# Kernel tuning notes

Measured on AMD Instinct MI355X. Metric: run time of the kernel, lower is better.

Reference implementation:

```python
import jax, jax.numpy as jnp
import numpy as np

N = 50000      # nodes
E = 800000     # edges (avg degree 16)
SIZES = [128, 128, 128, 128, 64]
NUM_LAYERS = 4


def setup_inputs() -> dict:
    key = jax.random.key(0)
    ks = jax.random.split(key, 3 + 2 * NUM_LAYERS)
    inp = {
        "x": jax.random.normal(ks[0], (N, SIZES[0]), dtype=jnp.float32),
        "edge_index": jax.random.randint(ks[1], (2, E), 0, N, dtype=jnp.int64),
        "edge_weight": jax.random.uniform(ks[2], (E,), dtype=jnp.float32),
    }
    for i in range(NUM_LAYERS):
        fan_in = SIZES[i]
        inp[f"W{i}"] = (jax.random.normal(ks[3 + 2 * i], (SIZES[i], SIZES[i + 1]), dtype=jnp.float32)
                        / np.float32(np.sqrt(fan_in)))
        inp[f"b{i}"] = jnp.zeros((SIZES[i + 1],), dtype=jnp.float32)
    return inp


def gcn_conv(x, src, dst, ew, W, b, n):
    """PyG GCNConv with add_self_loops=True, normalize=True (eval mode).
    deg[i] = sum of incoming edge weights at i + 1 (self loop weight 1).
    norm(j->i) = deg[j]^-1/2 * w_ji * deg[i]^-1/2.
    Self loop contributes deg[i]^-1 * (xW)[i].
    """
    xw = x @ W                                                    # [n, out]
    deg = jax.ops.segment_sum(ew, dst, num_segments=n) + 1.0      # [n]
    dinv = jnp.where(deg > 0, jax.lax.rsqrt(deg), 0.0)            # deg^-1/2
    norm = dinv[src] * ew * dinv[dst]                             # [E]
    agg = jax.ops.segment_sum(xw[src] * norm[:, None], dst, num_segments=n)
    return agg + xw * (dinv * dinv)[:, None] + b


def reference(x, edge_index, edge_weight, W0, b0, W1, b1, W2, b2, W3, b3):
    # Dropout p=0.5 is identity in eval mode (training=False).
    src, dst = edge_index[0], edge_index[1]
    Ws = [W0, W1, W2, W3]
    bs = [b0, b1, b2, b3]
    for i in range(NUM_LAYERS):
        x = gcn_conv(x, src, dst, edge_weight, Ws[i], bs[i], N)
        if i < NUM_LAYERS - 1:
            x = jax.nn.relu(x)
    return x
```

## Files before the change

kernel.cpp:

```cpp
#include <hip/hip_runtime.h>
#include <hip/hip_fp16.h>


#define DEG_SCALE 4194304.0f
#define BCAP 5120
#define K1_EDGES 4096
#define ACT_LD 136

using f16x8 = __attribute__((ext_vector_type(8))) _Float16;
using f32x4 = __attribute__((ext_vector_type(4))) float;

__global__ void prep_kernel(const float* __restrict__ W0, const float* __restrict__ W1,
                            const float* __restrict__ W2, const float* __restrict__ W3,
                            __half* P0, __half* P1, __half* P2, __half* P3,
                            int* gCursor, int nBuckets) {
    int blk = blockIdx.x;
    if (blk == 28) {
        int t = threadIdx.x;
        if (t < nBuckets) gCursor[t] = t * BCAP;
        return;
    }
    int t = blk * 256 + threadIdx.x;
    const float* W;
    __half* P;
    int OUT;
    if (t < 2048)      { W = W0; P = P0; OUT = 128; }
    else if (t < 4096) { W = W1; P = P1; OUT = 128; t -= 2048; }
    else if (t < 6144) { W = W2; P = P2; OUT = 128; t -= 4096; }
    else               { W = W3; P = P3; OUT = 64;  t -= 6144; }
    int lane = t & 63, fi = t >> 6;
    int nt = fi >> 2, kc = fi & 3;
    int col = 16 * nt + (lane & 15);
    int k0  = 32 * kc + 8 * (lane >> 4);
    union { __half h[8]; uint4 u; } v;
#pragma unroll
    for (int j = 0; j < 8; j++) v.h[j] = __float2half_rn(W[(size_t)(k0 + j) * OUT + col]);
    *(uint4*)&P[((size_t)fi * 64 + lane) * 8] = v.u;
}

__global__ __launch_bounds__(256) void bucket_scatter_kernel(
        const int* __restrict__ src, const int* __restrict__ dst,
        const float* __restrict__ ew, int* gCursor,
        int2* __restrict__ bucketArr, int E, int nBuckets) {
    __shared__ int cnt[256];
    __shared__ int runBase[256];
    int tid = threadIdx.x;
    int e0 = blockIdx.x * K1_EDGES;
    int e1 = min(e0 + K1_EDGES, E);
    cnt[tid] = 0;
    __syncthreads();
    for (int e = e0 + tid; e < e1; e += 256)
        atomicAdd(&cnt[dst[e] >> 8], 1);
    __syncthreads();
    if (tid < nBuckets && cnt[tid] > 0)
        runBase[tid] = atomicAdd(&gCursor[tid], cnt[tid]);
    __syncthreads();
    cnt[tid] = 0;
    __syncthreads();
    for (int e = e0 + tid; e < e1; e += 256) {
        int d = dst[e];
        int b = d >> 8;
        int slot = runBase[b] + atomicAdd(&cnt[b], 1);
        if (slot < (b + 1) * BCAP)
            bucketArr[slot] = make_int2((src[e] & 0xFFFF) | (d << 16),
                                        __float_as_int(ew[e]));
    }
}

__global__ __launch_bounds__(256) void bucket_csr_kernel(
        const int2* __restrict__ bucketArr, const int* __restrict__ gCursor,
        int2* __restrict__ epack, int* __restrict__ row_ptr,
        float* __restrict__ dinv, int N, int E, int nBuckets) {
    __shared__ int2 st[BCAP];
    __shared__ int cnt[256];
    __shared__ int scn[256];
    __shared__ int cur[256];
    __shared__ unsigned int dfix[256];
    __shared__ int cbase_sh;
    int b   = blockIdx.x;
    int tid = threadIdx.x;
    int node0 = b << 8;
    int nloc  = min(256, N - node0);
    int base  = b * BCAP;

    int sz = (tid < nBuckets) ? (gCursor[tid] - tid * BCAP) : 0;
    scn[tid] = sz;
    __syncthreads();
    for (int off = 1; off < 256; off <<= 1) {
        int u = (tid >= off) ? scn[tid - off] : 0;
        __syncthreads();
        scn[tid] += u;
        __syncthreads();
    }
    if (tid == b) cbase_sh = scn[tid] - sz;
    cnt[tid]  = 0;
    dfix[tid] = 0u;
    __syncthreads();
    int cbase = cbase_sh;
    int size  = gCursor[b] - base;

    for (int i = tid; i < size; i += 256) {
        int2 v = bucketArr[base + i];
        st[i] = v;
        int dl = (v.x >> 16) & 255;
        atomicAdd(&cnt[dl], 1);
        atomicAdd(&dfix[dl], (unsigned int)rintf(__int_as_float(v.y) * DEG_SCALE));
    }
    __syncthreads();

    if (tid < nloc) {
        float d = (float)dfix[tid] * (1.0f / DEG_SCALE) + 1.0f;
        dinv[node0 + tid] = rsqrtf(d);
    }

    int val = cnt[tid];
    scn[tid] = val;
    __syncthreads();
    for (int off = 1; off < 256; off <<= 1) {
        int u = (tid >= off) ? scn[tid - off] : 0;
        __syncthreads();
        scn[tid] += u;
        __syncthreads();
    }
    int excl = scn[tid] - val;
    scn[tid] = excl;
    if (tid < nloc) row_ptr[node0 + tid] = cbase + excl;
    if (b == nBuckets - 1 && tid == 0) row_ptr[N] = E;
    cur[tid] = 0;
    __syncthreads();

    for (int i = tid; i < size; i += 256) {
        int2 v = st[i];
        int dl = (v.x >> 16) & 255;
        int p  = cbase + scn[dl] + atomicAdd(&cur[dl], 1);
        epack[p] = make_int2(v.x & 0xFFFF, v.y);
    }
}

__global__ __launch_bounds__(256) void gemm0_kernel(const float* __restrict__ x,
                                                    const __half* __restrict__ Wpack,
                                                    const float* __restrict__ dinv,
                                                    __half* __restrict__ xw, int nrows) {
    constexpr int OUT = 128, NT = 8, CPR = 16;
    __shared__ __half D[64 * OUT];
    int tid  = threadIdx.x;
    int wave = tid >> 6, lane = tid & 63;
    int r = lane & 15, g = lane >> 4;
    int row0 = blockIdx.x * 64 + wave * 16;

    int arow = row0 + r;
    if (arow >= nrows) arow = nrows - 1;

    f16x8 a[4];
#pragma unroll
    for (int kc = 0; kc < 4; kc++) {
        const float* p = x + (size_t)arow * 128 + kc * 32 + g * 8;
        float4 u = *(const float4*)p;
        float4 v = *(const float4*)(p + 4);
        a[kc][0] = (_Float16)u.x; a[kc][1] = (_Float16)u.y;
        a[kc][2] = (_Float16)u.z; a[kc][3] = (_Float16)u.w;
        a[kc][4] = (_Float16)v.x; a[kc][5] = (_Float16)v.y;
        a[kc][6] = (_Float16)v.z; a[kc][7] = (_Float16)v.w;
    }

    float4 dv = *(const float4*)&dinv[row0 + 4 * g];

#pragma unroll
    for (int nt = 0; nt < NT; nt++) {
        const f16x8* Bp = (const f16x8*)(Wpack) + (size_t)nt * 4 * 64 + lane;
        f32x4 c = {0.f, 0.f, 0.f, 0.f};
        c = __builtin_amdgcn_mfma_f32_16x16x32_f16(a[0], Bp[0],   c, 0, 0, 0);
        c = __builtin_amdgcn_mfma_f32_16x16x32_f16(a[1], Bp[64],  c, 0, 0, 0);
        c = __builtin_amdgcn_mfma_f32_16x16x32_f16(a[2], Bp[128], c, 0, 0, 0);
        c = __builtin_amdgcn_mfma_f32_16x16x32_f16(a[3], Bp[192], c, 0, 0, 0);
        c[0] *= dv.x; c[1] *= dv.y; c[2] *= dv.z; c[3] *= dv.w;
        int col = 16 * nt + r;
#pragma unroll
        for (int j = 0; j < 4; j++) {
            int drow = wave * 16 + 4 * g + j;
            int ch   = (col >> 3) ^ (drow & (CPR - 1));
            D[drow * OUT + ch * 8 + (col & 7)] = __float2half_rn(c[j]);
        }
    }
    __syncthreads();
#pragma unroll
    for (int i = 0; i < 4; i++) {
        int idx  = tid + i * 256;
        int drow = idx / CPR;
        int ch   = idx % CPR;
        int gr   = blockIdx.x * 64 + drow;
        if (gr < nrows) {
            f16x8 v = *(f16x8*)&D[drow * OUT + ((ch ^ (drow & (CPR - 1))) << 3)];
            *(f16x8*)&xw[(size_t)gr * OUT + ch * 8] = v;
        }
    }
}

template <int OUT_NEXT>
__global__ __launch_bounds__(256) void gather_gemm_kernel(
        const __half* __restrict__ xwh,
        const int* __restrict__ rp,
        const int2* __restrict__ epack,
        const float* __restrict__ dinv,
        const float* __restrict__ bias,
        const __half* __restrict__ Wpack,
        __half* __restrict__ xw_out,
        int n) {
    constexpr int NT  = OUT_NEXT / 16;
    constexpr int CPR = OUT_NEXT / 8;
    __shared__ __half actAll[4 * 16 * ACT_LD];
    int tid  = threadIdx.x;
    int wv   = tid >> 6, lane = tid & 63;
    __half* act = &actAll[wv * 16 * ACT_LD];
    int node0 = blockIdx.x * 64 + wv * 16;

    for (int lrow = 0; lrow < 16; lrow++) {
        int node = node0 + lrow;
        if (node >= n) continue;
        node = __builtin_amdgcn_readfirstlane(node);
        int e0 = rp[node], e1 = rp[node + 1];
        float ax = 0.f, ay = 0.f;
        int e = e0;
        for (; e + 8 <= e1; e += 8) {
            int2 v0 = epack[e + 0], v1 = epack[e + 1], v2 = epack[e + 2], v3 = epack[e + 3];
            int2 v4 = epack[e + 4], v5 = epack[e + 5], v6 = epack[e + 6], v7 = epack[e + 7];
            __half2 h0 = ((const __half2*)(xwh + (size_t)v0.x * 128))[lane];
            __half2 h1 = ((const __half2*)(xwh + (size_t)v1.x * 128))[lane];
            __half2 h2 = ((const __half2*)(xwh + (size_t)v2.x * 128))[lane];
            __half2 h3 = ((const __half2*)(xwh + (size_t)v3.x * 128))[lane];
            __half2 h4 = ((const __half2*)(xwh + (size_t)v4.x * 128))[lane];
            __half2 h5 = ((const __half2*)(xwh + (size_t)v5.x * 128))[lane];
            __half2 h6 = ((const __half2*)(xwh + (size_t)v6.x * 128))[lane];
            __half2 h7 = ((const __half2*)(xwh + (size_t)v7.x * 128))[lane];
            float w0 = __int_as_float(v0.y), w1 = __int_as_float(v1.y);
            float w2 = __int_as_float(v2.y), w3 = __int_as_float(v3.y);
            float w4 = __int_as_float(v4.y), w5 = __int_as_float(v5.y);
            float w6 = __int_as_float(v6.y), w7 = __int_as_float(v7.y);
            ax += __half2float(h0.x) * w0 + __half2float(h1.x) * w1
                + __half2float(h2.x) * w2 + __half2float(h3.x) * w3
                + __half2float(h4.x) * w4 + __half2float(h5.x) * w5
                + __half2float(h6.x) * w6 + __half2float(h7.x) * w7;
            ay += __half2float(h0.y) * w0 + __half2float(h1.y) * w1
                + __half2float(h2.y) * w2 + __half2float(h3.y) * w3
                + __half2float(h4.y) * w4 + __half2float(h5.y) * w5
                + __half2float(h6.y) * w6 + __half2float(h7.y) * w7;
        }
        for (; e + 2 <= e1; e += 2) {
            int2 v0 = epack[e + 0], v1 = epack[e + 1];
            __half2 h0 = ((const __half2*)(xwh + (size_t)v0.x * 128))[lane];
            __half2 h1 = ((const __half2*)(xwh + (size_t)v1.x * 128))[lane];
            float w0 = __int_as_float(v0.y), w1 = __int_as_float(v1.y);
            ax += __half2float(h0.x) * w0 + __half2float(h1.x) * w1;
            ay += __half2float(h0.y) * w0 + __half2float(h1.y) * w1;
        }
        for (; e < e1; e++) {
            int2 v = epack[e];
            __half2 h = ((const __half2*)(xwh + (size_t)v.x * 128))[lane];
            float w = __int_as_float(v.y);
            ax += __half2float(h.x) * w;
            ay += __half2float(h.y) * w;
        }
        float   dvn = dinv[node];
        __half2 hs  = ((const __half2*)(xwh + (size_t)node * 128))[lane];
        float2  bl  = *(const float2*)&bias[lane * 2];
        float ox = fmaxf(dvn * (ax + __half2float(hs.x)) + bl.x, 0.f);
        float oy = fmaxf(dvn * (ay + __half2float(hs.y)) + bl.y, 0.f);
        __half2 ho;
        ho.x = __float2half_rn(ox);
        ho.y = __float2half_rn(oy);
        *(__half2*)&act[lrow * ACT_LD + lane * 2] = ho;
    }

    int r = lane & 15, g = lane >> 4;
    f16x8 a[4];
#pragma unroll
    for (int kc = 0; kc < 4; kc++)
        a[kc] = *(const f16x8*)&act[r * ACT_LD + kc * 32 + g * 8];

    float4 dvw = *(const float4*)&dinv[node0 + 4 * g];

#pragma unroll
    for (int nt = 0; nt < NT; nt++) {
        const f16x8* Bp = (const f16x8*)(Wpack) + (size_t)nt * 4 * 64 + lane;
        f32x4 c = {0.f, 0.f, 0.f, 0.f};
        c = __builtin_amdgcn_mfma_f32_16x16x32_f16(a[0], Bp[0],   c, 0, 0, 0);
        c = __builtin_amdgcn_mfma_f32_16x16x32_f16(a[1], Bp[64],  c, 0, 0, 0);
        c = __builtin_amdgcn_mfma_f32_16x16x32_f16(a[2], Bp[128], c, 0, 0, 0);
        c = __builtin_amdgcn_mfma_f32_16x16x32_f16(a[3], Bp[192], c, 0, 0, 0);
        c[0] *= dvw.x; c[1] *= dvw.y; c[2] *= dvw.z; c[3] *= dvw.w;
        int col = 16 * nt + r;
#pragma unroll
        for (int j = 0; j < 4; j++) {
            int drow = 4 * g + j;
            int ch   = (col >> 3) ^ (drow & (CPR - 1));
            act[drow * OUT_NEXT + ch * 8 + (col & 7)] = __float2half_rn(c[j]);
        }
    }

#pragma unroll
    for (int i = 0; i < 16 * CPR / 64; i++) {
        int idx  = lane + i * 64;
        int drow = idx / CPR;
        int ch   = idx % CPR;
        int gr   = node0 + drow;
        if (gr < n) {
            f16x8 v = *(f16x8*)&act[drow * OUT_NEXT + ((ch ^ (drow & (CPR - 1))) << 3)];
            *(f16x8*)&xw_out[(size_t)gr * OUT_NEXT + ch * 8] = v;
        }
    }
}

__global__ __launch_bounds__(256) void gather64h_kernel(const __half* __restrict__ xwh,
                                                        const int* __restrict__ rp,
                                                        const int2* __restrict__ epack,
                                                        const float* __restrict__ dinv,
                                                        const float* __restrict__ bias,
                                                        float* __restrict__ out, int n) {
    int lane = threadIdx.x & 63;
    int node = (blockIdx.x * blockDim.x + threadIdx.x) >> 6;
    if (node >= n) return;
    node = __builtin_amdgcn_readfirstlane(node);
    int e0 = rp[node], e1 = rp[node + 1];
    float acc = 0.f;

    int e = e0;
    for (; e + 8 <= e1; e += 8) {
        int2 v0 = epack[e + 0], v1 = epack[e + 1], v2 = epack[e + 2], v3 = epack[e + 3];
        int2 v4 = epack[e + 4], v5 = epack[e + 5], v6 = epack[e + 6], v7 = epack[e + 7];
        float r0 = __half2float(xwh[(size_t)v0.x * 64 + lane]);
        float r1 = __half2float(xwh[(size_t)v1.x * 64 + lane]);
        float r2 = __half2float(xwh[(size_t)v2.x * 64 + lane]);
        float r3 = __half2float(xwh[(size_t)v3.x * 64 + lane]);
        float r4 = __half2float(xwh[(size_t)v4.x * 64 + lane]);
        float r5 = __half2float(xwh[(size_t)v5.x * 64 + lane]);
        float r6 = __half2float(xwh[(size_t)v6.x * 64 + lane]);
        float r7 = __half2float(xwh[(size_t)v7.x * 64 + lane]);
        acc += r0 * __int_as_float(v0.y) + r1 * __int_as_float(v1.y)
             + r2 * __int_as_float(v2.y) + r3 * __int_as_float(v3.y)
             + r4 * __int_as_float(v4.y) + r5 * __int_as_float(v5.y)
             + r6 * __int_as_float(v6.y) + r7 * __int_as_float(v7.y);
    }
    for (; e < e1; e++) {
        int2 v = epack[e];
        acc += __half2float(xwh[(size_t)v.x * 64 + lane]) * __int_as_float(v.y);
    }

    float self = __half2float(xwh[(size_t)node * 64 + lane]);
    out[(size_t)node * 64 + lane] = dinv[node] * (acc + self) + bias[lane];
}

extern "C" void kernel_launch(void* const* d_in, const int* in_sizes, int n_in,
                              void* d_out, int out_size, void* d_ws, size_t ws_size,
                              hipStream_t stream) {
    const float* x  = (const float*)d_in[0];
    const int*   ei = (const int*)d_in[1];
    const float* ew = (const float*)d_in[2];
    const float* W[4] = {(const float*)d_in[3], (const float*)d_in[5],
                         (const float*)d_in[7], (const float*)d_in[9]};
    const float* b[4] = {(const float*)d_in[4], (const float*)d_in[6],
                         (const float*)d_in[8], (const float*)d_in[10]};
    const int N = in_sizes[0] / 128;
    const int E = in_sizes[2];
    const int* srcIdx = ei;
    const int* dstIdx = ei + E;
    float* out = (float*)d_out;

    const int nBuckets = (N + 255) / 256;

    char* p = (char*)d_ws;
    auto alloc = [&](size_t bytes) -> char* {
        char* q = p;
        p += (bytes + 255) / 256 * 256;
        return q;
    };
    float*  dinv      = (float*)alloc((size_t)(N + 64) * 4);
    int*    row_ptr   = (int*)alloc((size_t)(N + 1) * 4);
    int*    gCursor   = (int*)alloc(256 * 4);
    int2*   bucketArr = (int2*)alloc((size_t)nBuckets * BCAP * 8);
    int2*   epack     = (int2*)alloc((size_t)E * 8);
    __half* xwA       = (__half*)alloc((size_t)N * 128 * 2);
    __half* xwB       = (__half*)alloc((size_t)N * 128 * 2);
    __half* Wp[4];
    Wp[0] = (__half*)alloc(128 * 128 * 2);
    Wp[1] = (__half*)alloc(128 * 128 * 2);
    Wp[2] = (__half*)alloc(128 * 128 * 2);
    Wp[3] = (__half*)alloc(128 * 64 * 2);

    const int k1_grid    = (E + K1_EDGES - 1) / K1_EDGES;
    const int gemm_grid  = (N + 63) / 64;
    const int fused_grid = (N + 63) / 64;
    const int g64_grid   = (N + 3) / 4;

    prep_kernel<<<29, 256, 0, stream>>>(W[0], W[1], W[2], W[3],
                                        Wp[0], Wp[1], Wp[2], Wp[3],
                                        gCursor, nBuckets);
    bucket_scatter_kernel<<<k1_grid, 256, 0, stream>>>(srcIdx, dstIdx, ew, gCursor,
                                                       bucketArr, E, nBuckets);
    bucket_csr_kernel<<<nBuckets, 256, 0, stream>>>(bucketArr, gCursor, epack,
                                                    row_ptr, dinv, N, E, nBuckets);
    gemm0_kernel<<<gemm_grid, 256, 0, stream>>>(x, Wp[0], dinv, xwA, N);
    gather_gemm_kernel<128><<<fused_grid, 256, 0, stream>>>(
        xwA, row_ptr, epack, dinv, b[0], Wp[1], xwB, N);
    gather_gemm_kernel<128><<<fused_grid, 256, 0, stream>>>(
        xwB, row_ptr, epack, dinv, b[1], Wp[2], xwA, N);
    gather_gemm_kernel<64><<<fused_grid, 256, 0, stream>>>(
        xwA, row_ptr, epack, dinv, b[2], Wp[3], xwB, N);
    gather64h_kernel<<<g64_grid, 256, 0, stream>>>(
        xwB, row_ptr, epack, dinv, b[3], out, N);
}
```

Baseline: 226.5 us.

## Split gather-GEMM block work across waves: 16 nodes per block, shared MFMA tile

Each block now covers 16 nodes instead of 64. Each wave gathers 4 node rows into one shared activation tile, then each wave computes a slice of the output column tiles with MFMA, and a separate staging buffer holds the result. The grid grows fourfold, which adds parallelism and balances load across CUs. Per-wave serial gather latency drops from 16 nodes to 4. In exchange it adds two block barriers and makes every wave reload the A fragments redundantly.

```diff
diff --git a/kernel.cpp b/kernel.cpp
--- a/kernel.cpp
+++ b/kernel.cpp
@@ -207,69 +207,74 @@
         __half* __restrict__ xw_out,
         int n) {
     constexpr int NT  = OUT_NEXT / 16;
+    constexpr int NTW = NT / 4;
     constexpr int CPR = OUT_NEXT / 8;
-    __shared__ __half actAll[4 * 16 * ACT_LD];
+    __shared__ __half act[16 * ACT_LD];
+    __shared__ __half D[16 * OUT_NEXT];
     int tid  = threadIdx.x;
     int wv   = tid >> 6, lane = tid & 63;
-    __half* act = &actAll[wv * 16 * ACT_LD];
-    int node0 = blockIdx.x * 64 + wv * 16;
-
-    for (int lrow = 0; lrow < 16; lrow++) {
+    int node0 = blockIdx.x * 16;
+
+#pragma unroll
+    for (int k = 0; k < 4; k++) {
+        int lrow = wv * 4 + k;
         int node = node0 + lrow;
-        if (node >= n) continue;
-        node = __builtin_amdgcn_readfirstlane(node);
-        int e0 = rp[node], e1 = rp[node + 1];
-        float ax = 0.f, ay = 0.f;
-        int e = e0;
-        for (; e + 8 <= e1; e += 8) {
-            int2 v0 = epack[e + 0], v1 = epack[e + 1], v2 = epack[e + 2], v3 = epack[e + 3];
-            int2 v4 = epack[e + 4], v5 = epack[e + 5], v6 = epack[e + 6], v7 = epack[e + 7];
-            __half2 h0 = ((const __half2*)(xwh + (size_t)v0.x * 128))[lane];
-            __half2 h1 = ((const __half2*)(xwh + (size_t)v1.x * 128))[lane];
-            __half2 h2 = ((const __half2*)(xwh + (size_t)v2.x * 128))[lane];
-            __half2 h3 = ((const __half2*)(xwh + (size_t)v3.x * 128))[lane];
-            __half2 h4 = ((const __half2*)(xwh + (size_t)v4.x * 128))[lane];
-            __half2 h5 = ((const __half2*)(xwh + (size_t)v5.x * 128))[lane];
-            __half2 h6 = ((const __half2*)(xwh + (size_t)v6.x * 128))[lane];
-            __half2 h7 = ((const __half2*)(xwh + (size_t)v7.x * 128))[lane];
-            float w0 = __int_as_float(v0.y), w1 = __int_as_float(v1.y);
-            float w2 = __int_as_float(v2.y), w3 = __int_as_float(v3.y);
-            float w4 = __int_as_float(v4.y), w5 = __int_as_float(v5.y);
-            float w6 = __int_as_float(v6.y), w7 = __int_as_float(v7.y);
-            ax += __half2float(h0.x) * w0 + __half2float(h1.x) * w1
-                + __half2float(h2.x) * w2 + __half2float(h3.x) * w3
-                + __half2float(h4.x) * w4 + __half2float(h5.x) * w5
-                + __half2float(h6.x) * w6 + __half2float(h7.x) * w7;
-            ay += __half2float(h0.y) * w0 + __half2float(h1.y) * w1
-                + __half2float(h2.y) * w2 + __half2float(h3.y) * w3
-                + __half2float(h4.y) * w4 + __half2float(h5.y) * w5
-                + __half2float(h6.y) * w6 + __half2float(h7.y) * w7;
+        if (node < n) {
+            node = __builtin_amdgcn_readfirstlane(node);
+            int e0 = rp[node], e1 = rp[node + 1];
+            float ax = 0.f, ay = 0.f;
+            int e = e0;
+            for (; e + 8 <= e1; e += 8) {
+                int2 v0 = epack[e + 0], v1 = epack[e + 1], v2 = epack[e + 2], v3 = epack[e + 3];
+                int2 v4 = epack[e + 4], v5 = epack[e + 5], v6 = epack[e + 6], v7 = epack[e + 7];
+                __half2 h0 = ((const __half2*)(xwh + (size_t)v0.x * 128))[lane];
+                __half2 h1 = ((const __half2*)(xwh + (size_t)v1.x * 128))[lane];
+                __half2 h2 = ((const __half2*)(xwh + (size_t)v2.x * 128))[lane];
+                __half2 h3 = ((const __half2*)(xwh + (size_t)v3.x * 128))[lane];
+                __half2 h4 = ((const __half2*)(xwh + (size_t)v4.x * 128))[lane];
+                __half2 h5 = ((const __half2*)(xwh + (size_t)v5.x * 128))[lane];
+                __half2 h6 = ((const __half2*)(xwh + (size_t)v6.x * 128))[lane];
+                __half2 h7 = ((const __half2*)(xwh + (size_t)v7.x * 128))[lane];
+                float w0 = __int_as_float(v0.y), w1 = __int_as_float(v1.y);
+                float w2 = __int_as_float(v2.y), w3 = __int_as_float(v3.y);
+                float w4 = __int_as_float(v4.y), w5 = __int_as_float(v5.y);
+                float w6 = __int_as_float(v6.y), w7 = __int_as_float(v7.y);
+                ax += __half2float(h0.x) * w0 + __half2float(h1.x) * w1
+                    + __half2float(h2.x) * w2 + __half2float(h3.x) * w3
+                    + __half2float(h4.x) * w4 + __half2float(h5.x) * w5
+                    + __half2float(h6.x) * w6 + __half2float(h7.x) * w7;
+                ay += __half2float(h0.y) * w0 + __half2float(h1.y) * w1
+                    + __half2float(h2.y) * w2 + __half2float(h3.y) * w3
+                    + __half2float(h4.y) * w4 + __half2float(h5.y) * w5
+                    + __half2float(h6.y) * w6 + __half2float(h7.y) * w7;
+            }
+            for (; e + 2 <= e1; e += 2) {
+                int2 v0 = epack[e + 0], v1 = epack[e + 1];
+                __half2 h0 = ((const __half2*)(xwh + (size_t)v0.x * 128))[lane];
+                __half2 h1 = ((const __half2*)(xwh + (size_t)v1.x * 128))[lane];
+                float w0 = __int_as_float(v0.y), w1 = __int_as_float(v1.y);
+                ax += __half2float(h0.x) * w0 + __half2float(h1.x) * w1;
+                ay += __half2float(h0.y) * w0 + __half2float(h1.y) * w1;
+            }
+            for (; e < e1; e++) {
+                int2 v = epack[e];
+                __half2 h = ((const __half2*)(xwh + (size_t)v.x * 128))[lane];
+                float w = __int_as_float(v.y);
+                ax += __half2float(h.x) * w;
+                ay += __half2float(h.y) * w;
+            }
+            float   dvn = dinv[node];
+            __half2 hs  = ((const __half2*)(xwh + (size_t)node * 128))[lane];
+            float2  bl  = *(const float2*)&bias[lane * 2];
+            float ox = fmaxf(dvn * (ax + __half2float(hs.x)) + bl.x, 0.f);
+            float oy = fmaxf(dvn * (ay + __half2float(hs.y)) + bl.y, 0.f);
+            __half2 ho;
+            ho.x = __float2half_rn(ox);
+            ho.y = __float2half_rn(oy);
+            *(__half2*)&act[lrow * ACT_LD + lane * 2] = ho;
         }
-        for (; e + 2 <= e1; e += 2) {
-            int2 v0 = epack[e + 0], v1 = epack[e + 1];
-            __half2 h0 = ((const __half2*)(xwh + (size_t)v0.x * 128))[lane];
-            __half2 h1 = ((const __half2*)(xwh + (size_t)v1.x * 128))[lane];
-            float w0 = __int_as_float(v0.y), w1 = __int_as_float(v1.y);
-            ax += __half2float(h0.x) * w0 + __half2float(h1.x) * w1;
-            ay += __half2float(h0.y) * w0 + __half2float(h1.y) * w1;
-        }
-        for (; e < e1; e++) {
-            int2 v = epack[e];
-            __half2 h = ((const __half2*)(xwh + (size_t)v.x * 128))[lane];
-            float w = __int_as_float(v.y);
-            ax += __half2float(h.x) * w;
-            ay += __half2float(h.y) * w;
-        }
-        float   dvn = dinv[node];
-        __half2 hs  = ((const __half2*)(xwh + (size_t)node * 128))[lane];
-        float2  bl  = *(const float2*)&bias[lane * 2];
-        float ox = fmaxf(dvn * (ax + __half2float(hs.x)) + bl.x, 0.f);
-        float oy = fmaxf(dvn * (ay + __half2float(hs.y)) + bl.y, 0.f);
-        __half2 ho;
-        ho.x = __float2half_rn(ox);
-        ho.y = __float2half_rn(oy);
-        *(__half2*)&act[lrow * ACT_LD + lane * 2] = ho;
-    }
+    }
+    __syncthreads();
 
     int r = lane & 15, g = lane >> 4;
     f16x8 a[4];
@@ -280,7 +285,8 @@
     float4 dvw = *(const float4*)&dinv[node0 + 4 * g];
 
 #pragma unroll
-    for (int nt = 0; nt < NT; nt++) {
+    for (int t = 0; t < NTW; t++) {
+        int nt = wv * NTW + t;
         const f16x8* Bp = (const f16x8*)(Wpack) + (size_t)nt * 4 * 64 + lane;
         f32x4 c = {0.f, 0.f, 0.f, 0.f};
         c = __builtin_amdgcn_mfma_f32_16x16x32_f16(a[0], Bp[0],   c, 0, 0, 0);
@@ -293,18 +299,18 @@
         for (int j = 0; j < 4; j++) {
             int drow = 4 * g + j;
             int ch   = (col >> 3) ^ (drow & (CPR - 1));
-            act[drow * OUT_NEXT + ch * 8 + (col & 7)] = __float2half_rn(c[j]);
+            D[drow * OUT_NEXT + ch * 8 + (col & 7)] = __float2half_rn(c[j]);
         }
     }
-
-#pragma unroll
-    for (int i = 0; i < 16 * CPR / 64; i++) {
-        int idx  = lane + i * 64;
-        int drow = idx / CPR;
-        int ch   = idx % CPR;
+    __syncthreads();
+
+    constexpr int CHUNKS = 16 * CPR;
+    if (tid < CHUNKS) {
+        int drow = tid / CPR;
+        int ch   = tid % CPR;
         int gr   = node0 + drow;
         if (gr < n) {
-            f16x8 v = *(f16x8*)&act[drow * OUT_NEXT + ((ch ^ (drow & (CPR - 1))) << 3)];
+            f16x8 v = *(f16x8*)&D[drow * OUT_NEXT + ((ch ^ (drow & (CPR - 1))) << 3)];
             *(f16x8*)&xw_out[(size_t)gr * OUT_NEXT + ch * 8] = v;
         }
     }
@@ -388,7 +394,7 @@
 
     const int k1_grid    = (E + K1_EDGES - 1) / K1_EDGES;
     const int gemm_grid  = (N + 63) / 64;
-    const int fused_grid = (N + 63) / 64;
+    const int fused_grid = (N + 15) / 16;
     const int g64_grid   = (N + 3) / 4;
 
     prep_kernel<<<29, 256, 0, stream>>>(W[0], W[1], W[2], W[3],
```

Result: faster. 190.6 us (-15.9%).
